# Optimization experiments

Measured on AMD Instinct MI355X. Metric: run time of the kernel, lower is better.

Reference implementation:

```python
import jax, jax.numpy as jnp
import numpy as np

N_NODES = 50000
N_EDGES = 800000
H = 4


def setup_inputs() -> dict:
    key = jax.random.key(0)
    ks = jax.random.split(key, 12)
    s = 0.05
    return {
        "x_feat": jax.random.normal(ks[0], (N_NODES, 128), jnp.float32),
        "W_fc": jax.random.normal(ks[1], (128, 256), jnp.float32) * s,
        "W1": jax.random.normal(ks[2], (256, 256), jnp.float32) * s,
        "al1": jax.random.normal(ks[3], (H, 64), jnp.float32) * s,
        "ar1": jax.random.normal(ks[4], (H, 64), jnp.float32) * s,
        "b1": jnp.zeros((256,), jnp.float32),
        "W2": jax.random.normal(ks[5], (256, 256), jnp.float32) * s,
        "al2": jax.random.normal(ks[6], (H, 64), jnp.float32) * s,
        "ar2": jax.random.normal(ks[7], (H, 64), jnp.float32) * s,
        "b2": jnp.zeros((256,), jnp.float32),
        "src": jax.random.randint(ks[8], (N_EDGES,), 0, N_NODES, jnp.int64 if jax.config.jax_enable_x64 else jnp.int32),
        "dst": jax.random.randint(ks[9], (N_EDGES,), 0, N_NODES, jnp.int64 if jax.config.jax_enable_x64 else jnp.int32),
    }


def _gat_layer(x, src, dst, W, attn_l, attn_r, bias, n_nodes):
    """DGL GATConv: project, per-edge leaky-relu scores, edge softmax by dst,
    weighted segment-sum, + bias, ELU. Returns [N, H, dh]."""
    h, dh = attn_l.shape
    feat = (x @ W).reshape(n_nodes, h, dh)            # [N,H,dh]
    el = jnp.einsum('nhd,hd->nh', feat, attn_l)        # [N,H]
    er = jnp.einsum('nhd,hd->nh', feat, attn_r)        # [N,H]
    e = jax.nn.leaky_relu(el[src] + er[dst], 0.2)      # [E,H]
    # numerically stable segment softmax over incoming edges of each dst
    m = jax.ops.segment_max(e, dst, num_segments=n_nodes)
    ex = jnp.exp(e - m[dst])
    z = jax.ops.segment_sum(ex, dst, num_segments=n_nodes)
    a = ex / z[dst]                                    # [E,H]
    msg = feat[src] * a[:, :, None]                    # [E,H,dh]
    out = jax.ops.segment_sum(msg, dst, num_segments=n_nodes)  # [N,H,dh]
    out = out + bias.reshape(h, dh)
    return jax.nn.elu(out)


def reference(x_feat, W_fc, W1, al1, ar1, b1, W2, al2, ar2, b2, src, dst):
    n = x_feat.shape[0]
    h = jnp.tanh(x_feat @ W_fc)                         # [N,256] (dropout = identity in eval)
    g1 = _gat_layer(h, src, dst, W1, al1, ar1, b1, n)   # [N,4,64]
    g1 = g1.reshape(n, -1)                              # [N,256]
    g2 = _gat_layer(g1, src, dst, W2, al2, ar2, b2, n)  # [N,4,64]
    return jnp.mean(g2, axis=-2)                        # mean over heads -> [N,64]
```

## Files before the change

### kernel.cpp

```cpp
#include <hip/hip_runtime.h>
#include <hip/hip_bf16.h>
#include <hip/hip_fp16.h>
#include <math.h>


typedef __attribute__((ext_vector_type(8))) short bf16x8;
typedef __attribute__((ext_vector_type(4))) float f32x4;

__device__ __forceinline__ void split2(float v, short& h, short& l) {
    __hip_bfloat16 bh = __float2bfloat16(v);
    float r = v - __bfloat162float(bh);
    __hip_bfloat16 bl = __float2bfloat16(r);
    h = *reinterpret_cast<short*>(&bh);
    l = *reinterpret_cast<short*>(&bl);
}

__device__ __forceinline__ float fast_tanh(float x) {
    x = fminf(fmaxf(x, -15.f), 15.f);
    float e = __expf(2.f * x);
    return (e - 1.f) * __builtin_amdgcn_rcpf(e + 1.f);
}

__device__ __forceinline__ float leaky02(float x) { return x > 0.f ? x : 0.2f * x; }

__device__ __forceinline__ float sel_head(float4 q, int h) {
    float lo = (h & 1) ? q.y : q.x;
    float hi = (h & 1) ? q.w : q.z;
    return (h & 2) ? hi : lo;
}

__global__ __launch_bounds__(256) void wsplit3_kernel(
        const float* __restrict__ W0, short* __restrict__ B0h, short* __restrict__ B0l,
        const float* __restrict__ W1, short* __restrict__ B1h, short* __restrict__ B1l,
        const float* __restrict__ W2, short* __restrict__ B2h, short* __restrict__ B2l) {
    int idx = blockIdx.x * 256 + threadIdx.x;
    const float* W;
    short *Bh, *Bl;
    int K, rel;
    if (idx < 128 * 256) {
        W = W0; Bh = B0h; Bl = B0l; K = 128; rel = idx;
    } else if (idx < 128 * 256 + 256 * 256) {
        W = W1; Bh = B1h; Bl = B1l; K = 256; rel = idx - 128 * 256;
    } else if (idx < 128 * 256 + 2 * 256 * 256) {
        W = W2; Bh = B2h; Bl = B2l; K = 256; rel = idx - 128 * 256 - 256 * 256;
    } else {
        return;
    }
    int k = rel >> 8, n = rel & 255;
    short h, l;
    split2(W[rel], h, l);
    Bh[n * K + k] = h;
    Bl[n * K + k] = l;
}

template<bool TANH, bool ELER, bool HALF_OUT>
__global__ __launch_bounds__(256, 2) void mfma_gemm_kernel(
        const float* __restrict__ A, const short* __restrict__ Bh,
        const short* __restrict__ Bl, float* __restrict__ C,
        __half* __restrict__ C16, int M, int K,
        const float* __restrict__ al, const float* __restrict__ ar,
        float* __restrict__ el, float* __restrict__ er) {
    __shared__ __align__(16) short As_h[128 * 32];
    __shared__ __align__(16) short As_l[128 * 32];
    __shared__ __align__(16) short Bs_h[128 * 32];
    __shared__ __align__(16) short Bs_l[128 * 32];

    const int tid = threadIdx.x;
    const int row0 = blockIdx.x * 128;
    const int col0 = blockIdx.y * 128;

    const int sr = tid >> 1;
    const int sc = (tid & 1) << 4;

    const int lane = tid & 63;
    const int lr = lane & 15;
    const int lg = lane >> 4;
    const int wid = tid >> 6;
    const int wm = wid >> 1;
    const int wn = wid & 1;

    f32x4 acc[4][4];
#pragma unroll
    for (int i = 0; i < 4; ++i)
#pragma unroll
        for (int j = 0; j < 4; ++j) acc[i][j] = (f32x4){0.f, 0.f, 0.f, 0.f};

    for (int k0 = 0; k0 < K; k0 += 32) {
        {
            float va[16];
            int g = row0 + sr;
            if (g < M) {
                const float4* ap = reinterpret_cast<const float4*>(&A[(size_t)g * K + k0 + sc]);
#pragma unroll
                for (int i = 0; i < 4; ++i) *reinterpret_cast<float4*>(&va[i * 4]) = ap[i];
            } else {
#pragma unroll
                for (int i = 0; i < 16; ++i) va[i] = 0.f;
            }
            short hs[16], ls[16];
#pragma unroll
            for (int i = 0; i < 16; ++i) split2(va[i], hs[i], ls[i]);
            *reinterpret_cast<bf16x8*>(&As_h[sr * 32 + sc])     = *reinterpret_cast<bf16x8*>(&hs[0]);
            *reinterpret_cast<bf16x8*>(&As_h[sr * 32 + sc + 8]) = *reinterpret_cast<bf16x8*>(&hs[8]);
            *reinterpret_cast<bf16x8*>(&As_l[sr * 32 + sc])     = *reinterpret_cast<bf16x8*>(&ls[0]);
            *reinterpret_cast<bf16x8*>(&As_l[sr * 32 + sc + 8]) = *reinterpret_cast<bf16x8*>(&ls[8]);
        }
        {
            const short* bhp = &Bh[(size_t)(col0 + sr) * K + k0 + sc];
            const short* blp = &Bl[(size_t)(col0 + sr) * K + k0 + sc];
            *reinterpret_cast<bf16x8*>(&Bs_h[sr * 32 + sc])     = *reinterpret_cast<const bf16x8*>(bhp);
            *reinterpret_cast<bf16x8*>(&Bs_h[sr * 32 + sc + 8]) = *reinterpret_cast<const bf16x8*>(bhp + 8);
            *reinterpret_cast<bf16x8*>(&Bs_l[sr * 32 + sc])     = *reinterpret_cast<const bf16x8*>(blp);
            *reinterpret_cast<bf16x8*>(&Bs_l[sr * 32 + sc + 8]) = *reinterpret_cast<const bf16x8*>(blp + 8);
        }
        __syncthreads();

        bf16x8 ah[4], av[4], bh[4], bv[4];
#pragma unroll
        for (int t = 0; t < 4; ++t) {
            int arow = (wm * 64 + t * 16 + lr) * 32 + lg * 8;
            int brow = (wn * 64 + t * 16 + lr) * 32 + lg * 8;
            ah[t] = *reinterpret_cast<const bf16x8*>(&As_h[arow]);
            av[t] = *reinterpret_cast<const bf16x8*>(&As_l[arow]);
            bh[t] = *reinterpret_cast<const bf16x8*>(&Bs_h[brow]);
            bv[t] = *reinterpret_cast<const bf16x8*>(&Bs_l[brow]);
        }
#pragma unroll
        for (int mt = 0; mt < 4; ++mt)
#pragma unroll
            for (int nt = 0; nt < 4; ++nt) {
                acc[mt][nt] = __builtin_amdgcn_mfma_f32_16x16x32_bf16(ah[mt], bh[nt], acc[mt][nt], 0, 0, 0);
                acc[mt][nt] = __builtin_amdgcn_mfma_f32_16x16x32_bf16(ah[mt], bv[nt], acc[mt][nt], 0, 0, 0);
                acc[mt][nt] = __builtin_amdgcn_mfma_f32_16x16x32_bf16(av[mt], bh[nt], acc[mt][nt], 0, 0, 0);
            }
        __syncthreads();
    }

    const int head = blockIdx.y * 2 + wn;
    float alv[4], arv[4];
    if (ELER) {
#pragma unroll
        for (int nt = 0; nt < 4; ++nt) {
            alv[nt] = al[head * 64 + nt * 16 + lr];
            arv[nt] = ar[head * 64 + nt * 16 + lr];
        }
    }
#pragma unroll
    for (int mt = 0; mt < 4; ++mt) {
#pragma unroll
        for (int r = 0; r < 4; ++r) {
            int row = row0 + wm * 64 + mt * 16 + lg * 4 + r;
            bool valid = row < M;
            float sl = 0.f, sr_ = 0.f;
#pragma unroll
            for (int nt = 0; nt < 4; ++nt) {
                float v = acc[mt][nt][r];
                if (TANH) v = fast_tanh(v);
                if (valid) {
                    size_t ci = (size_t)row * 256 + col0 + wn * 64 + nt * 16 + lr;
                    if (HALF_OUT) C16[ci] = __float2half(v);
                    else          C[ci] = v;
                }
                if (ELER) { sl = fmaf(v, alv[nt], sl); sr_ = fmaf(v, arv[nt], sr_); }
            }
            if (ELER) {
#pragma unroll
                for (int mask = 1; mask < 16; mask <<= 1) {
                    sl  += __shfl_xor(sl, mask, 16);
                    sr_ += __shfl_xor(sr_, mask, 16);
                }
                if (valid && lr == 0) {
                    el[row * 4 + head] = sl;
                    er[row * 4 + head] = sr_;
                }
            }
        }
    }
}

__global__ void count_deg_kernel(const int* __restrict__ dst, int* __restrict__ deg, int E) {
    int i = blockIdx.x * blockDim.x + threadIdx.x;
    if (i < E) atomicAdd(&deg[dst[i]], 1);
}

__global__ __launch_bounds__(1024) void scan_kernel(const int* __restrict__ deg,
                                                    int* __restrict__ offs,
                                                    int* __restrict__ cursor, int n) {
    __shared__ int wsum[16];
    const int tid = threadIdx.x, lane = tid & 63, wv = tid >> 6;
    int carry = 0;
    for (int base = 0; base < n; base += 1024) {
        int i = base + tid;
        int v = (i < n) ? deg[i] : 0;
        int incl = v;
#pragma unroll
        for (int d = 1; d < 64; d <<= 1) {
            int t = __shfl_up(incl, d, 64);
            if (lane >= d) incl += t;
        }
        if (lane == 63) wsum[wv] = incl;
        __syncthreads();
        int woff = 0, tot = 0;
#pragma unroll
        for (int w2 = 0; w2 < 16; ++w2) {
            int s = wsum[w2];
            if (w2 < wv) woff += s;
            tot += s;
        }
        int excl = carry + woff + incl - v;
        if (i < n) { offs[i] = excl; cursor[i] = excl; }
        carry += tot;
        __syncthreads();
    }
    if (tid == 0) offs[n] = carry;
}

__global__ void fill_csr_kernel(const int* __restrict__ src, const int* __restrict__ dst,
                                int* __restrict__ cursor, int* __restrict__ srcs_sorted,
                                int* __restrict__ dsts_sorted, int E) {
    int i = blockIdx.x * blockDim.x + threadIdx.x;
    if (i < E) {
        int d = dst[i];
        int pos = atomicAdd(&cursor[d], 1);
        srcs_sorted[pos] = src[i];
        dsts_sorted[pos] = d;
    }
}

__global__ __launch_bounds__(256) void edge_w_kernel(const int* __restrict__ srcs,
                                                     const int* __restrict__ dsts,
                                                     const float* __restrict__ el,
                                                     const float* __restrict__ er,
                                                     float4* __restrict__ w, int E) {
    int i = blockIdx.x * 256 + threadIdx.x;
    if (i >= E) return;
    int s = srcs[i], d = dsts[i];
    const float4 a = *reinterpret_cast<const float4*>(&el[(size_t)s * 4]);
    const float4 b = *reinterpret_cast<const float4*>(&er[(size_t)d * 4]);
    float4 o;
    o.x = __expf(leaky02(a.x + b.x));
    o.y = __expf(leaky02(a.y + b.y));
    o.z = __expf(leaky02(a.z + b.z));
    o.w = __expf(leaky02(a.w + b.w));
    w[i] = o;
}

template<bool FINAL>
__global__ __launch_bounds__(256) void gat_agg_kernel(const __half* __restrict__ feat,
                                                      const float4* __restrict__ wq,
                                                      const int* __restrict__ srcs,
                                                      const int* __restrict__ offs,
                                                      const float* __restrict__ bias,
                                                      float* __restrict__ out, int N) {
    const int tid = threadIdx.x;
    const int w = tid >> 6, l = tid & 63;
    const int n = blockIdx.x * 4 + w;
    if (n >= N) return;
    const int h = l >> 4;
    const int begin = offs[n];
    const int deg = offs[n + 1] - begin;
    const __half* fbase = feat + (size_t)l * 4;
    const float4 zero4 = make_float4(0.f, 0.f, 0.f, 0.f);

    float4 acc = zero4;
    float z = 0.f;

    for (int j = 0; j < deg; j += 8) {
        const int rem = deg - j;
        const int nb = __builtin_amdgcn_readfirstlane(begin + j);
        const int s0 = srcs[nb + 0];
        const int s1 = (rem > 1) ? srcs[nb + 1] : 0;
        const int s2 = (rem > 2) ? srcs[nb + 2] : 0;
        const int s3 = (rem > 3) ? srcs[nb + 3] : 0;
        const int s4 = (rem > 4) ? srcs[nb + 4] : 0;
        const int s5 = (rem > 5) ? srcs[nb + 5] : 0;
        const int s6 = (rem > 6) ? srcs[nb + 6] : 0;
        const int s7 = (rem > 7) ? srcs[nb + 7] : 0;
        const float4 w0 = wq[nb + 0];
        const float4 w1 = (rem > 1) ? wq[nb + 1] : zero4;
        const float4 w2 = (rem > 2) ? wq[nb + 2] : zero4;
        const float4 w3 = (rem > 3) ? wq[nb + 3] : zero4;
        const float4 w4 = (rem > 4) ? wq[nb + 4] : zero4;
        const float4 w5 = (rem > 5) ? wq[nb + 5] : zero4;
        const float4 w6 = (rem > 6) ? wq[nb + 6] : zero4;
        const float4 w7 = (rem > 7) ? wq[nb + 7] : zero4;
        const uint2 u0 = *reinterpret_cast<const uint2*>(fbase + (size_t)s0 * 256);
        const uint2 u1 = *reinterpret_cast<const uint2*>(fbase + (size_t)s1 * 256);
        const uint2 u2 = *reinterpret_cast<const uint2*>(fbase + (size_t)s2 * 256);
        const uint2 u3 = *reinterpret_cast<const uint2*>(fbase + (size_t)s3 * 256);
        const uint2 u4 = *reinterpret_cast<const uint2*>(fbase + (size_t)s4 * 256);
        const uint2 u5 = *reinterpret_cast<const uint2*>(fbase + (size_t)s5 * 256);
        const uint2 u6 = *reinterpret_cast<const uint2*>(fbase + (size_t)s6 * 256);
        const uint2 u7 = *reinterpret_cast<const uint2*>(fbase + (size_t)s7 * 256);

        const float e0 = sel_head(w0, h);
        const float e1 = sel_head(w1, h);
        const float e2 = sel_head(w2, h);
        const float e3 = sel_head(w3, h);
        const float e4 = sel_head(w4, h);
        const float e5 = sel_head(w5, h);
        const float e6 = sel_head(w6, h);
        const float e7 = sel_head(w7, h);
        z += ((e0 + e1) + (e2 + e3)) + ((e4 + e5) + (e6 + e7));

        auto fma4 = [&](float e, uint2 u) {
            const __half2* hp = reinterpret_cast<const __half2*>(&u);
            float2 a = __half22float2(hp[0]);
            float2 b = __half22float2(hp[1]);
            acc.x = fmaf(e, a.x, acc.x); acc.y = fmaf(e, a.y, acc.y);
            acc.z = fmaf(e, b.x, acc.z); acc.w = fmaf(e, b.y, acc.w);
        };
        fma4(e0, u0); fma4(e1, u1); fma4(e2, u2); fma4(e3, u3);
        fma4(e4, u4); fma4(e5, u5); fma4(e6, u6); fma4(e7, u7);
    }

    const float rz = (z > 0.f) ? __builtin_amdgcn_rcpf(z) : 0.f;
    const float4 bv = *reinterpret_cast<const float4*>(&bias[l * 4]);
    float4 v;
    v.x = fmaf(acc.x, rz, bv.x);
    v.y = fmaf(acc.y, rz, bv.y);
    v.z = fmaf(acc.z, rz, bv.z);
    v.w = fmaf(acc.w, rz, bv.w);
    v.x = v.x > 0.f ? v.x : expm1f(v.x);
    v.y = v.y > 0.f ? v.y : expm1f(v.y);
    v.z = v.z > 0.f ? v.z : expm1f(v.z);
    v.w = v.w > 0.f ? v.w : expm1f(v.w);

    if (!FINAL) {
        *reinterpret_cast<float4*>(&out[(size_t)n * 256 + l * 4]) = v;
    } else {
        v.x += __shfl_down(v.x, 32, 64); v.y += __shfl_down(v.y, 32, 64);
        v.z += __shfl_down(v.z, 32, 64); v.w += __shfl_down(v.w, 32, 64);
        v.x += __shfl_down(v.x, 16, 64); v.y += __shfl_down(v.y, 16, 64);
        v.z += __shfl_down(v.z, 16, 64); v.w += __shfl_down(v.w, 16, 64);
        if (l < 16) {
            float4 o;
            o.x = 0.25f * v.x; o.y = 0.25f * v.y; o.z = 0.25f * v.z; o.w = 0.25f * v.w;
            *reinterpret_cast<float4*>(&out[(size_t)n * 64 + l * 4]) = o;
        }
    }
}

extern "C" void kernel_launch(void* const* d_in, const int* in_sizes, int n_in,
                              void* d_out, int out_size, void* d_ws, size_t ws_size,
                              hipStream_t stream) {
    const float* x_feat = (const float*)d_in[0];
    const float* W_fc   = (const float*)d_in[1];
    const float* W1     = (const float*)d_in[2];
    const float* al1    = (const float*)d_in[3];
    const float* ar1    = (const float*)d_in[4];
    const float* b1     = (const float*)d_in[5];
    const float* W2     = (const float*)d_in[6];
    const float* al2    = (const float*)d_in[7];
    const float* ar2    = (const float*)d_in[8];
    const float* b2     = (const float*)d_in[9];
    const int*   src    = (const int*)d_in[10];
    const int*   dst    = (const int*)d_in[11];
    float* out = (float*)d_out;

    const int N = in_sizes[0] / 128;
    const int E = in_sizes[10];

    char* ws = (char*)d_ws;
    size_t off = 0;
    auto alloc = [&](size_t bytes) -> void* {
        off = (off + 255) & ~(size_t)255;
        void* p = ws + off;
        off += bytes;
        return p;
    };
    float* buf0  = (float*)alloc((size_t)N * 256 * 4);
    __half* f16  = (__half*)alloc((size_t)N * 256 * 2);
    float* el    = (float*)alloc((size_t)N * 4 * 4);
    float* er    = (float*)alloc((size_t)N * 4 * 4);
    int* deg     = (int*)alloc((size_t)N * 4);
    int* offs    = (int*)alloc((size_t)(N + 1) * 4);
    int* cursor  = (int*)alloc((size_t)N * 4);
    int* srcs_sorted = (int*)alloc((size_t)(E + 8) * 4);
    int* dsts_sorted = (int*)alloc((size_t)(E + 8) * 4);
    float4* wq   = (float4*)alloc((size_t)(E + 8) * 16);
    short* Bfc_h = (short*)alloc((size_t)256 * 128 * 2);
    short* Bfc_l = (short*)alloc((size_t)256 * 128 * 2);
    short* B1_h  = (short*)alloc((size_t)256 * 256 * 2);
    short* B1_l  = (short*)alloc((size_t)256 * 256 * 2);
    short* B2_h  = (short*)alloc((size_t)256 * 256 * 2);
    short* B2_l  = (short*)alloc((size_t)256 * 256 * 2);

    const int eb = (E + 255) / 256;
    dim3 ggrid((N + 127) / 128, 2);
    const int agrid = (N + 3) / 4;

    hipMemsetAsync(deg, 0, (size_t)N * 4, stream);
    count_deg_kernel<<<eb, 256, 0, stream>>>(dst, deg, E);
    scan_kernel<<<1, 1024, 0, stream>>>(deg, offs, cursor, N);
    fill_csr_kernel<<<eb, 256, 0, stream>>>(src, dst, cursor, srcs_sorted, dsts_sorted, E);

    wsplit3_kernel<<<(128 * 256 + 2 * 256 * 256 + 255) / 256, 256, 0, stream>>>(
        W_fc, Bfc_h, Bfc_l, W1, B1_h, B1_l, W2, B2_h, B2_l);

    mfma_gemm_kernel<true, false, false><<<ggrid, 256, 0, stream>>>(
        x_feat, Bfc_h, Bfc_l, buf0, nullptr, N, 128, nullptr, nullptr, nullptr, nullptr);
    mfma_gemm_kernel<false, true, true><<<ggrid, 256, 0, stream>>>(
        buf0, B1_h, B1_l, nullptr, f16, N, 256, al1, ar1, el, er);
    edge_w_kernel<<<eb, 256, 0, stream>>>(srcs_sorted, dsts_sorted, el, er, wq, E);
    gat_agg_kernel<false><<<agrid, 256, 0, stream>>>(f16, wq, srcs_sorted, offs, b1, buf0, N);
    mfma_gemm_kernel<false, true, true><<<ggrid, 256, 0, stream>>>(
        buf0, B2_h, B2_l, nullptr, f16, N, 256, al2, ar2, el, er);
    edge_w_kernel<<<eb, 256, 0, stream>>>(srcs_sorted, dsts_sorted, el, er, wq, E);
    gat_agg_kernel<true><<<agrid, 256, 0, stream>>>(f16, wq, srcs_sorted, offs, b2, out, N);
}
```

Measured before the change: 463.3 us.

## Store intermediate activations pre-split into bf16 hi/lo pairs and vectorize scan

```diff
diff --git a/kernel.cpp b/kernel.cpp
--- a/kernel.cpp
+++ b/kernel.cpp
@@ -53,11 +53,23 @@
     Bl[n * K + k] = l;
 }
 
-template<bool TANH, bool ELER, bool HALF_OUT>
+__global__ __launch_bounds__(256) void xsplit_kernel(const float* __restrict__ X,
+                                                     short* __restrict__ Xh,
+                                                     short* __restrict__ Xl, int total) {
+    int idx = blockIdx.x * 256 + threadIdx.x;
+    if (idx >= total) return;
+    short h, l;
+    split2(X[idx], h, l);
+    Xh[idx] = h;
+    Xl[idx] = l;
+}
+
+template<bool TANH, bool ELER, bool SPLIT_OUT>
 __global__ __launch_bounds__(256, 2) void mfma_gemm_kernel(
-        const float* __restrict__ A, const short* __restrict__ Bh,
-        const short* __restrict__ Bl, float* __restrict__ C,
-        __half* __restrict__ C16, int M, int K,
+        const short* __restrict__ Ah, const short* __restrict__ Al,
+        const short* __restrict__ Bh, const short* __restrict__ Bl,
+        short* __restrict__ Oh, short* __restrict__ Ol, __half* __restrict__ O16,
+        int M, int K,
         const float* __restrict__ al, const float* __restrict__ ar,
         float* __restrict__ el, float* __restrict__ er) {
     __shared__ __align__(16) short As_h[128 * 32];
@@ -87,23 +99,12 @@
 
     for (int k0 = 0; k0 < K; k0 += 32) {
         {
-            float va[16];
-            int g = row0 + sr;
-            if (g < M) {
-                const float4* ap = reinterpret_cast<const float4*>(&A[(size_t)g * K + k0 + sc]);
-#pragma unroll
-                for (int i = 0; i < 4; ++i) *reinterpret_cast<float4*>(&va[i * 4]) = ap[i];
-            } else {
-#pragma unroll
-                for (int i = 0; i < 16; ++i) va[i] = 0.f;
-            }
-            short hs[16], ls[16];
-#pragma unroll
-            for (int i = 0; i < 16; ++i) split2(va[i], hs[i], ls[i]);
-            *reinterpret_cast<bf16x8*>(&As_h[sr * 32 + sc])     = *reinterpret_cast<bf16x8*>(&hs[0]);
-            *reinterpret_cast<bf16x8*>(&As_h[sr * 32 + sc + 8]) = *reinterpret_cast<bf16x8*>(&hs[8]);
-            *reinterpret_cast<bf16x8*>(&As_l[sr * 32 + sc])     = *reinterpret_cast<bf16x8*>(&ls[0]);
-            *reinterpret_cast<bf16x8*>(&As_l[sr * 32 + sc + 8]) = *reinterpret_cast<bf16x8*>(&ls[8]);
+            const short* ap_h = &Ah[(size_t)(row0 + sr) * K + k0 + sc];
+            const short* ap_l = &Al[(size_t)(row0 + sr) * K + k0 + sc];
+            *reinterpret_cast<bf16x8*>(&As_h[sr * 32 + sc])     = *reinterpret_cast<const bf16x8*>(ap_h);
+            *reinterpret_cast<bf16x8*>(&As_h[sr * 32 + sc + 8]) = *reinterpret_cast<const bf16x8*>(ap_h + 8);
+            *reinterpret_cast<bf16x8*>(&As_l[sr * 32 + sc])     = *reinterpret_cast<const bf16x8*>(ap_l);
+            *reinterpret_cast<bf16x8*>(&As_l[sr * 32 + sc + 8]) = *reinterpret_cast<const bf16x8*>(ap_l + 8);
         }
         {
             const short* bhp = &Bh[(size_t)(col0 + sr) * K + k0 + sc];
@@ -158,8 +159,14 @@
                 if (TANH) v = fast_tanh(v);
                 if (valid) {
                     size_t ci = (size_t)row * 256 + col0 + wn * 64 + nt * 16 + lr;
-                    if (HALF_OUT) C16[ci] = __float2half(v);
-                    else          C[ci] = v;
+                    if (SPLIT_OUT) {
+                        short hh, ll;
+                        split2(v, hh, ll);
+                        Oh[ci] = hh;
+                        Ol[ci] = ll;
+                    } else {
+                        O16[ci] = __float2half(v);
+                    }
                 }
                 if (ELER) { sl = fmaf(v, alv[nt], sl); sr_ = fmaf(v, arv[nt], sr_); }
             }
@@ -189,10 +196,19 @@
     __shared__ int wsum[16];
     const int tid = threadIdx.x, lane = tid & 63, wv = tid >> 6;
     int carry = 0;
-    for (int base = 0; base < n; base += 1024) {
-        int i = base + tid;
-        int v = (i < n) ? deg[i] : 0;
-        int incl = v;
+    for (int base = 0; base < n; base += 4096) {
+        int i = base + tid * 4;
+        int v0 = 0, v1 = 0, v2 = 0, v3 = 0;
+        if (i + 3 < n) {
+            int4 q = *reinterpret_cast<const int4*>(&deg[i]);
+            v0 = q.x; v1 = q.y; v2 = q.z; v3 = q.w;
+        } else if (i < n) {
+            v0 = deg[i];
+            if (i + 1 < n) v1 = deg[i + 1];
+            if (i + 2 < n) v2 = deg[i + 2];
+        }
+        int s = v0 + v1 + v2 + v3;
+        int incl = s;
 #pragma unroll
         for (int d = 1; d < 64; d <<= 1) {
             int t = __shfl_up(incl, d, 64);
@@ -203,12 +219,18 @@
         int woff = 0, tot = 0;
 #pragma unroll
         for (int w2 = 0; w2 < 16; ++w2) {
-            int s = wsum[w2];
-            if (w2 < wv) woff += s;
-            tot += s;
-        }
-        int excl = carry + woff + incl - v;
-        if (i < n) { offs[i] = excl; cursor[i] = excl; }
+            int x = wsum[w2];
+            if (w2 < wv) woff += x;
+            tot += x;
+        }
+        int excl = carry + woff + incl - s;
+        if (i < n) {
+            int p0 = excl, p1 = p0 + v0, p2 = p1 + v1, p3 = p2 + v2;
+            offs[i] = p0; cursor[i] = p0;
+            if (i + 1 < n) { offs[i + 1] = p1; cursor[i + 1] = p1; }
+            if (i + 2 < n) { offs[i + 2] = p2; cursor[i + 2] = p2; }
+            if (i + 3 < n) { offs[i + 3] = p3; cursor[i + 3] = p3; }
+        }
         carry += tot;
         __syncthreads();
     }
@@ -251,7 +273,9 @@
                                                       const int* __restrict__ srcs,
                                                       const int* __restrict__ offs,
                                                       const float* __restrict__ bias,
-                                                      float* __restrict__ out, int N) {
+                                                      float* __restrict__ out,
+                                                      short* __restrict__ Gh,
+                                                      short* __restrict__ Gl, int N) {
     const int tid = threadIdx.x;
     const int w = tid >> 6, l = tid & 63;
     const int n = blockIdx.x * 4 + w;
@@ -327,7 +351,13 @@
     v.w = v.w > 0.f ? v.w : expm1f(v.w);
 
     if (!FINAL) {
-        *reinterpret_cast<float4*>(&out[(size_t)n * 256 + l * 4]) = v;
+        short4 hh, ll;
+        split2(v.x, hh.x, ll.x);
+        split2(v.y, hh.y, ll.y);
+        split2(v.z, hh.z, ll.z);
+        split2(v.w, hh.w, ll.w);
+        *reinterpret_cast<short4*>(&Gh[(size_t)n * 256 + l * 4]) = hh;
+        *reinterpret_cast<short4*>(&Gl[(size_t)n * 256 + l * 4]) = ll;
     } else {
         v.x += __shfl_down(v.x, 32, 64); v.y += __shfl_down(v.y, 32, 64);
         v.z += __shfl_down(v.z, 32, 64); v.w += __shfl_down(v.w, 32, 64);
@@ -360,6 +390,8 @@
 
     const int N = in_sizes[0] / 128;
     const int E = in_sizes[10];
+    const int NB = (N + 127) / 128;
+    const int M_pad = NB * 128;
 
     char* ws = (char*)d_ws;
     size_t off = 0;
@@ -369,16 +401,19 @@
         off += bytes;
         return p;
     };
-    float* buf0  = (float*)alloc((size_t)N * 256 * 4);
-    __half* f16  = (__half*)alloc((size_t)N * 256 * 2);
-    float* el    = (float*)alloc((size_t)N * 4 * 4);
-    float* er    = (float*)alloc((size_t)N * 4 * 4);
-    int* deg     = (int*)alloc((size_t)N * 4);
-    int* offs    = (int*)alloc((size_t)(N + 1) * 4);
-    int* cursor  = (int*)alloc((size_t)N * 4);
+    short* Xh   = (short*)alloc((size_t)M_pad * 128 * 2);
+    short* Xl   = (short*)alloc((size_t)M_pad * 128 * 2);
+    short* Hh   = (short*)alloc((size_t)M_pad * 256 * 2);
+    short* Hl   = (short*)alloc((size_t)M_pad * 256 * 2);
+    __half* f16 = (__half*)alloc((size_t)M_pad * 256 * 2);
+    float* el   = (float*)alloc((size_t)N * 4 * 4);
+    float* er   = (float*)alloc((size_t)N * 4 * 4);
+    int* deg    = (int*)alloc((size_t)N * 4);
+    int* offs   = (int*)alloc((size_t)(N + 4) * 4);
+    int* cursor = (int*)alloc((size_t)N * 4);
     int* srcs_sorted = (int*)alloc((size_t)(E + 8) * 4);
     int* dsts_sorted = (int*)alloc((size_t)(E + 8) * 4);
-    float4* wq   = (float4*)alloc((size_t)(E + 8) * 16);
+    float4* wq  = (float4*)alloc((size_t)(E + 8) * 16);
     short* Bfc_h = (short*)alloc((size_t)256 * 128 * 2);
     short* Bfc_l = (short*)alloc((size_t)256 * 128 * 2);
     short* B1_h  = (short*)alloc((size_t)256 * 256 * 2);
@@ -387,7 +422,7 @@
     short* B2_l  = (short*)alloc((size_t)256 * 256 * 2);
 
     const int eb = (E + 255) / 256;
-    dim3 ggrid((N + 127) / 128, 2);
+    dim3 ggrid(NB, 2);
     const int agrid = (N + 3) / 4;
 
     hipMemsetAsync(deg, 0, (size_t)N * 4, stream);
@@ -397,15 +432,18 @@
 
     wsplit3_kernel<<<(128 * 256 + 2 * 256 * 256 + 255) / 256, 256, 0, stream>>>(
         W_fc, Bfc_h, Bfc_l, W1, B1_h, B1_l, W2, B2_h, B2_l);
-
-    mfma_gemm_kernel<true, false, false><<<ggrid, 256, 0, stream>>>(
-        x_feat, Bfc_h, Bfc_l, buf0, nullptr, N, 128, nullptr, nullptr, nullptr, nullptr);
-    mfma_gemm_kernel<false, true, true><<<ggrid, 256, 0, stream>>>(
-        buf0, B1_h, B1_l, nullptr, f16, N, 256, al1, ar1, el, er);
+    xsplit_kernel<<<(N * 128 + 255) / 256, 256, 0, stream>>>(x_feat, Xh, Xl, N * 128);
+
+    mfma_gemm_kernel<true, false, true><<<ggrid, 256, 0, stream>>>(
+        Xh, Xl, Bfc_h, Bfc_l, Hh, Hl, nullptr, N, 128, nullptr, nullptr, nullptr, nullptr);
+    mfma_gemm_kernel<false, true, false><<<ggrid, 256, 0, stream>>>(
+        Hh, Hl, B1_h, B1_l, nullptr, nullptr, f16, N, 256, al1, ar1, el, er);
     edge_w_kernel<<<eb, 256, 0, stream>>>(srcs_sorted, dsts_sorted, el, er, wq, E);
-    gat_agg_kernel<false><<<agrid, 256, 0, stream>>>(f16, wq, srcs_sorted, offs, b1, buf0, N);
-    mfma_gemm_kernel<false, true, true><<<ggrid, 256, 0, stream>>>(
-        buf0, B2_h, B2_l, nullptr, f16, N, 256, al2, ar2, el, er);
+    gat_agg_kernel<false><<<agrid, 256, 0, stream>>>(
+        f16, wq, srcs_sorted, offs, b1, nullptr, Hh, Hl, N);
+    mfma_gemm_kernel<false, true, false><<<ggrid, 256, 0, stream>>>(
+        Hh, Hl, B2_h, B2_l, nullptr, nullptr, f16, N, 256, al2, ar2, el, er);
     edge_w_kernel<<<eb, 256, 0, stream>>>(srcs_sorted, dsts_sorted, el, er, wq, E);
-    gat_agg_kernel<true><<<agrid, 256, 0, stream>>>(f16, wq, srcs_sorted, offs, b2, out, N);
-}
+    gat_agg_kernel<true><<<agrid, 256, 0, stream>>>(
+        f16, wq, srcs_sorted, offs, b2, out, nullptr, nullptr, N);
+}
```

Result: slower. 473.0 us (+2.1%).
